# Kernel optimization log

Measured on AMD Instinct MI355X. Metric: run time of the kernel, lower is better.

## Reference

```python
import jax, jax.numpy as jnp
import numpy as np

EPS = 1e-12  # matches torch F.normalize default eps

def l2norm(t):
    n = jnp.linalg.norm(t, axis=-1, keepdims=True)
    return t / jnp.maximum(n, EPS)

def rotate_half(x):
    # '... (j d) -> ... j d' with j=2: split into two halves, return cat(-x2, x1)
    x1, x2 = jnp.split(x, 2, axis=-1)
    return jnp.concatenate((-x2, x1), axis=-1)

def rotary_freqs(seq_len, dim):
    inv_freq = 1.0 / (10000.0 ** (jnp.arange(0, dim, 2, dtype=jnp.float32) / dim))
    seq = jnp.arange(seq_len, dtype=jnp.float32)
    freqs = seq[:, None] * inv_freq[None, :]          # [n, d/2]
    emb = jnp.concatenate((freqs, freqs), axis=-1)    # [n, d]
    return emb[None, None]                            # [1, 1, n, d]

def apply_rotary_pos_emb(t, freqs):
    # rot_dim == dim_head here, so the pass-through slice is empty
    return t * jnp.cos(freqs) + rotate_half(t) * jnp.sin(freqs)

def setup_inputs() -> dict:
    key = jax.random.key(0)
    kq, kk, kv = jax.random.split(key, 3)
    b, h, n, d = 2, 16, 2048, 64
    q = jax.random.normal(kq, (b, h, n, d), dtype=jnp.float32)
    k = jax.random.normal(kk, (b, h, n, d), dtype=jnp.float32)
    v = jax.random.normal(kv, (b, h, n, d), dtype=jnp.float32)
    q_scale = jnp.ones((d,), dtype=jnp.float32)
    k_scale = jnp.ones((d,), dtype=jnp.float32)
    return {"q": q, "k": k, "v": v, "q_scale": q_scale, "k_scale": k_scale}

def reference(q, k, v, q_scale, k_scale):
    b, h, n, d = q.shape
    # QK RMSNorm (l2 normalize + learned per-dim scale)
    q = l2norm(q) * q_scale
    k = l2norm(k) * k_scale
    # rotary position embedding (always applied in the source module)
    freqs = rotary_freqs(n, d)
    q = apply_rotary_pos_emb(q, freqs)
    k = apply_rotary_pos_emb(k, freqs)
    # attention: explicit scores -> softmax -> values
    scale = d ** -0.5
    sim = jnp.einsum('bhid,bhjd->bhij', q, k) * scale
    attn = jax.nn.softmax(sim, axis=-1)
    out = jnp.einsum('bhij,bhjd->bhid', attn, v)
    # 'b h n d -> b n (h d)'
    return out.transpose(0, 2, 1, 3).reshape(b, n, h * d)
```

## Files before the change

### kernel.cpp

```cpp
#include <hip/hip_runtime.h>
#include <math.h>

#define BH   32
#define NSEQ 2048
#define DH   64
#define NH   16
#define LOG2E 1.44269504088896f

typedef _Float16 f16x8 __attribute__((ext_vector_type(8)));
typedef __fp16   fp16x2 __attribute__((ext_vector_type(2)));
typedef float    f32x16v __attribute__((ext_vector_type(16)));

#if __has_builtin(__builtin_amdgcn_exp2f)
#define EXP2F(x) __builtin_amdgcn_exp2f(x)
#else
#define EXP2F(x) exp2f(x)
#endif

static __device__ __forceinline__ unsigned pkrtz(float a, float b) {
    fp16x2 r = __builtin_amdgcn_cvt_pkrtz(a, b);
    return __builtin_bit_cast(unsigned, r);
}
static __device__ __forceinline__ unsigned packh_rne(float a, float b) {
    union { _Float16 h[2]; unsigned u; } x;
    x.h[0] = (_Float16)a; x.h[1] = (_Float16)b;
    return x.u;
}
#if __has_builtin(__builtin_amdgcn_perm)
#define PERM(a, b, s) __builtin_amdgcn_perm((a), (b), (s))
#else
static __device__ __forceinline__ unsigned PERM(unsigned a, unsigned b, unsigned s) {
    if (s == 0x05040100u) return (b & 0xffffu) | (a << 16);
    return (b >> 16) | (a & 0xffff0000u);
}
#endif

static __device__ __forceinline__ float2 rope_cs(int pos, int p) {
    float invf_rev = EXP2F(-(float)p * (13.287712379549449f / 32.0f)) * 0.15915494309189535f;
    float rev = (float)pos * invf_rev;
    float fr = rev - floorf(rev);
    float th = fr * 6.283185307179586f;
    return make_float2(__cosf(th), __sinf(th));
}

__global__ __launch_bounds__(256) void prep_all(
    const float* __restrict__ q, const float* __restrict__ k, const float* __restrict__ v,
    const float* __restrict__ qs, const float* __restrict__ ksc,
    unsigned* __restrict__ qh, unsigned* __restrict__ kh, unsigned* __restrict__ vt2) {
    const int bid = blockIdx.x;
    const int t = threadIdx.x;
    if (bid < 16384) {
        const bool isq = bid < 8192;
        const float* in = isq ? q : k;
        const float* sc = isq ? qs : ksc;
        unsigned* outp  = isq ? qh : kh;
        const float smul = isq ? 0.125f * LOG2E : 1.0f;
        const int sb = bid & 8191;
        const int w = t >> 6, lane = t & 63;
        const int c = lane & 31, hfr = lane >> 5;
        const int row = sb * 8 + w * 2 + hfr;
        float2 x2 = *(const float2*)(in + (size_t)row * DH + 2 * c);
        float ss = x2.x * x2.x + x2.y * x2.y;
        #pragma unroll
        for (int off = 16; off > 0; off >>= 1) ss += __shfl_xor(ss, off);
        float inv = 1.0f / fmaxf(sqrtf(ss), 1e-12f);
        float2 s2 = *(const float2*)(sc + 2 * c);
        float t0 = x2.x * inv * s2.x;
        float t1 = x2.y * inv * s2.y;
        float p0 = __shfl_xor(t0, 16);
        float p1 = __shfl_xor(t1, 16);
        float r0 = (c < 16) ? -p0 : p0;
        float r1 = (c < 16) ? -p1 : p1;
        int pos = row & (NSEQ - 1);
        int pp = (2 * c) & 31;
        float2 cs0 = rope_cs(pos, pp);
        float2 cs1 = rope_cs(pos, pp + 1);
        float o0 = (t0 * cs0.x + r0 * cs0.y) * smul;
        float o1 = (t1 * cs1.x + r1 * cs1.y) * smul;
        outp[row * 32 + c] = packh_rne(o0, o1);
    } else {
        const int sb = bid - 16384;
        const int kt = sb & 31, bh = sb >> 5;
        __shared__ float Lv[64 * 68];
        #pragma unroll
        for (int i = 0; i < 4; ++i) {
            int chunk = t + 256 * i;
            int r = chunk >> 4, fg = chunk & 15;
            *(float4*)&Lv[r * 68 + fg * 4] =
                *(const float4*)(v + ((size_t)bh * NSEQ + kt * 64 + r) * DH + fg * 4);
        }
        __syncthreads();
        const int dp = t >> 3, kg = t & 7;
        unsigned u[8];
        #pragma unroll
        for (int j = 0; j < 8; ++j) {
            int key = kg * 8 + j;
            float2 f2 = *(const float2*)&Lv[key * 68 + 2 * dp];
            u[j] = pkrtz(f2.x, f2.y);
        }
        unsigned* dst = vt2 + ((size_t)bh * 32 + dp) * NSEQ + kt * 64 + kg * 8;
        *(uint4*)(dst + 0) = make_uint4(u[0], u[1], u[2], u[3]);
        *(uint4*)(dst + 4) = make_uint4(u[4], u[5], u[6], u[7]);
    }
}

__global__ __launch_bounds__(128, 2) void attn_kernel(
    const unsigned* __restrict__ qh, const unsigned* __restrict__ khg,
    const unsigned* __restrict__ vt2, float* __restrict__ out) {

    __shared__ _Float16 Ks[2][64 * 72];
    __shared__ _Float16 Vs[2][64 * 72];

    const int bh = blockIdx.y, qb = blockIdx.x;
    const int tid = threadIdx.x;
    const int w = tid >> 6, lane = tid & 63;
    const int c = lane & 31, hf = lane >> 5;

    const _Float16* qbase = (const _Float16*)qh + ((size_t)bh * NSEQ + qb * 64) * DH;
    const _Float16* kbase = (const _Float16*)khg + (size_t)bh * NSEQ * DH;
    const unsigned* vbase = vt2 + (size_t)bh * 32 * NSEQ;

    #pragma unroll
    for (int i = 0; i < 4; ++i) {
        int chunk = tid + 128 * i;
        int r = chunk >> 3, sg = chunk & 7;
        *(uint4*)&Ks[0][r * 72 + sg * 8] = *(const uint4*)(kbase + r * DH + sg * 8);
    }
    #pragma unroll
    for (int i = 0; i < 4; ++i) {
        int chunk = tid + 128 * i;
        int dp = chunk >> 4, kq = (chunk & 15) * 4;
        uint4 vr = *(const uint4*)(vbase + (size_t)dp * NSEQ + kq);
        uint2 lo, hi;
        lo.x = PERM(vr.y, vr.x, 0x05040100u); hi.x = PERM(vr.y, vr.x, 0x07060302u);
        lo.y = PERM(vr.w, vr.z, 0x05040100u); hi.y = PERM(vr.w, vr.z, 0x07060302u);
        *(uint2*)&Vs[0][(2 * dp) * 72 + kq]     = lo;
        *(uint2*)&Vs[0][(2 * dp + 1) * 72 + kq] = hi;
    }

    f16x8 qf[4];
    #pragma unroll
    for (int ks = 0; ks < 4; ++ks)
        qf[ks] = *(const f16x8*)(qbase + (w * 32 + c) * DH + ks * 16 + hf * 8);

    f32x16v o[2];
    #pragma unroll
    for (int mt = 0; mt < 2; ++mt)
        #pragma unroll
        for (int r = 0; r < 16; ++r) o[mt][r] = 0.f;
    float lpart = 0.f;

    __syncthreads();

    for (int jt = 0; jt < 32; ++jt) {
        const int cur = jt & 1;
        uint4 kpre[4], vpre[4];
        if (jt + 1 < 32) {
            #pragma unroll
            for (int i = 0; i < 4; ++i) {
                int chunk = tid + 128 * i;
                int r = chunk >> 3, sg = chunk & 7;
                kpre[i] = *(const uint4*)(kbase + (size_t)(jt + 1) * 64 * DH + r * DH + sg * 8);
            }
            #pragma unroll
            for (int i = 0; i < 4; ++i) {
                int chunk = tid + 128 * i;
                int dp = chunk >> 4, kq = (chunk & 15) * 4;
                vpre[i] = *(const uint4*)(vbase + (size_t)dp * NSEQ + (jt + 1) * 64 + kq);
            }
        }

        f32x16v s[2];
        #pragma unroll
        for (int mt = 0; mt < 2; ++mt)
            #pragma unroll
            for (int r = 0; r < 16; ++r) s[mt][r] = 0.f;
        #pragma unroll
        for (int ks = 0; ks < 4; ++ks) {
            f16x8 ka0 = *(const f16x8*)&Ks[cur][c * 72 + ks * 16 + hf * 8];
            f16x8 ka1 = *(const f16x8*)&Ks[cur][(32 + c) * 72 + ks * 16 + hf * 8];
            s[0] = __builtin_amdgcn_mfma_f32_32x32x16_f16(ka0, qf[ks], s[0], 0, 0, 0);
            s[1] = __builtin_amdgcn_mfma_f32_32x32x16_f16(ka1, qf[ks], s[1], 0, 0, 0);
        }

        #pragma unroll
        for (int mt = 0; mt < 2; ++mt)
            #pragma unroll
            for (int r = 0; r < 16; ++r) {
                float pv = EXP2F(s[mt][r]);
                s[mt][r] = pv;
                lpart += pv;
            }

        #pragma unroll
        for (int mt = 0; mt < 2; ++mt) {
            #pragma unroll
            for (int kk = 0; kk < 2; ++kk) {
                unsigned P01 = pkrtz(s[mt][kk * 8 + 0], s[mt][kk * 8 + 1]);
                unsigned P23 = pkrtz(s[mt][kk * 8 + 2], s[mt][kk * 8 + 3]);
                unsigned P45 = pkrtz(s[mt][kk * 8 + 4], s[mt][kk * 8 + 5]);
                unsigned P67 = pkrtz(s[mt][kk * 8 + 6], s[mt][kk * 8 + 7]);
                unsigned x01 = (unsigned)__shfl_xor((int)P01, 32);
                unsigned x23 = (unsigned)__shfl_xor((int)P23, 32);
                unsigned x45 = (unsigned)__shfl_xor((int)P45, 32);
                unsigned x67 = (unsigned)__shfl_xor((int)P67, 32);
                union { unsigned u[4]; f16x8 v; } B;
                B.u[0] = hf ? x45 : P01;
                B.u[1] = hf ? x67 : P23;
                B.u[2] = hf ? P45 : x01;
                B.u[3] = hf ? P67 : x23;
                const int kc = mt * 2 + kk;
                f16x8 va0 = *(const f16x8*)&Vs[cur][c * 72 + kc * 16 + hf * 8];
                f16x8 va1 = *(const f16x8*)&Vs[cur][(32 + c) * 72 + kc * 16 + hf * 8];
                o[0] = __builtin_amdgcn_mfma_f32_32x32x16_f16(va0, B.v, o[0], 0, 0, 0);
                o[1] = __builtin_amdgcn_mfma_f32_32x32x16_f16(va1, B.v, o[1], 0, 0, 0);
            }
        }

        if (jt + 1 < 32) {
            #pragma unroll
            for (int i = 0; i < 4; ++i) {
                int chunk = tid + 128 * i;
                int r = chunk >> 3, sg = chunk & 7;
                *(uint4*)&Ks[1 - cur][r * 72 + sg * 8] = kpre[i];
            }
            #pragma unroll
            for (int i = 0; i < 4; ++i) {
                int chunk = tid + 128 * i;
                int dp = chunk >> 4, kq = (chunk & 15) * 4;
                uint2 lo, hi;
                lo.x = PERM(vpre[i].y, vpre[i].x, 0x05040100u); hi.x = PERM(vpre[i].y, vpre[i].x, 0x07060302u);
                lo.y = PERM(vpre[i].w, vpre[i].z, 0x05040100u); hi.y = PERM(vpre[i].w, vpre[i].z, 0x07060302u);
                *(uint2*)&Vs[1 - cur][(2 * dp) * 72 + kq]     = lo;
                *(uint2*)&Vs[1 - cur][(2 * dp + 1) * 72 + kq] = hi;
            }
        }
        __syncthreads();
    }

    float ltot = lpart + __shfl_xor(lpart, 32);
    float invl = 1.0f / ltot;
    const int b = bh >> 4, h = bh & 15;
    const int pos = qb * 64 + w * 32 + c;
    float* obase = out + ((size_t)b * NSEQ + pos) * (NH * DH) + h * DH;
    #pragma unroll
    for (int mt = 0; mt < 2; ++mt)
        #pragma unroll
        for (int g = 0; g < 4; ++g) {
            float4 r4 = make_float4(o[mt][g * 4 + 0] * invl, o[mt][g * 4 + 1] * invl,
                                    o[mt][g * 4 + 2] * invl, o[mt][g * 4 + 3] * invl);
            *(float4*)(obase + mt * 32 + g * 8 + hf * 4) = r4;
        }
}

extern "C" void kernel_launch(void* const* d_in, const int* in_sizes, int n_in,
                              void* d_out, int out_size, void* d_ws, size_t ws_size,
                              hipStream_t stream) {
    const float* q  = (const float*)d_in[0];
    const float* k  = (const float*)d_in[1];
    const float* v  = (const float*)d_in[2];
    const float* qs = (const float*)d_in[3];
    const float* ks = (const float*)d_in[4];
    float* outp = (float*)d_out;

    unsigned* qh  = (unsigned*)d_ws;
    unsigned* kh  = qh + (size_t)BH * NSEQ * 32;
    unsigned* vt2 = kh + (size_t)BH * NSEQ * 32;

    prep_all<<<17408, 256, 0, stream>>>(q, k, v, qs, ks, qh, kh, vt2);
    attn_kernel<<<dim3(NSEQ / 64, BH), 128, 0, stream>>>(qh, kh, vt2, outp);
}
```

Before: 153.6 us.

## Split key tiles across four waves with LDS reduction of partial outputs

Doubles the block to four waves. Each pair of waves processes half of every key tile for the same query rows, and the partial O and row sums are combined through shared memory at the end. This shortens each wave's serial MFMA/exp chain per tile and adds more waves for latency hiding. The cost is duplicated Q fragments and O accumulators, plus an extra reduction pass. The cross-half exchange of P also switches to permlane32_swap when available.

```diff
diff --git a/kernel.cpp b/kernel.cpp
--- a/kernel.cpp
+++ b/kernel.cpp
@@ -10,6 +10,7 @@
 typedef _Float16 f16x8 __attribute__((ext_vector_type(8)));
 typedef __fp16   fp16x2 __attribute__((ext_vector_type(2)));
 typedef float    f32x16v __attribute__((ext_vector_type(16)));
+typedef unsigned uint2v __attribute__((ext_vector_type(2)));
 
 #if __has_builtin(__builtin_amdgcn_exp2f)
 #define EXP2F(x) __builtin_amdgcn_exp2f(x)
@@ -104,7 +105,7 @@
     }
 }
 
-__global__ __launch_bounds__(128, 2) void attn_kernel(
+__global__ __launch_bounds__(256, 4) void attn_kernel(
     const unsigned* __restrict__ qh, const unsigned* __restrict__ khg,
     const unsigned* __restrict__ vt2, float* __restrict__ out) {
 
@@ -115,20 +116,22 @@
     const int tid = threadIdx.x;
     const int w = tid >> 6, lane = tid & 63;
     const int c = lane & 31, hf = lane >> 5;
+    const int qhw = w & 1;
+    const int khw = w >> 1;
 
     const _Float16* qbase = (const _Float16*)qh + ((size_t)bh * NSEQ + qb * 64) * DH;
     const _Float16* kbase = (const _Float16*)khg + (size_t)bh * NSEQ * DH;
     const unsigned* vbase = vt2 + (size_t)bh * 32 * NSEQ;
 
     #pragma unroll
-    for (int i = 0; i < 4; ++i) {
-        int chunk = tid + 128 * i;
+    for (int i = 0; i < 2; ++i) {
+        int chunk = tid + 256 * i;
         int r = chunk >> 3, sg = chunk & 7;
         *(uint4*)&Ks[0][r * 72 + sg * 8] = *(const uint4*)(kbase + r * DH + sg * 8);
     }
     #pragma unroll
-    for (int i = 0; i < 4; ++i) {
-        int chunk = tid + 128 * i;
+    for (int i = 0; i < 2; ++i) {
+        int chunk = tid + 256 * i;
         int dp = chunk >> 4, kq = (chunk & 15) * 4;
         uint4 vr = *(const uint4*)(vbase + (size_t)dp * NSEQ + kq);
         uint2 lo, hi;
@@ -141,7 +144,7 @@
     f16x8 qf[4];
     #pragma unroll
     for (int ks = 0; ks < 4; ++ks)
-        qf[ks] = *(const f16x8*)(qbase + (w * 32 + c) * DH + ks * 16 + hf * 8);
+        qf[ks] = *(const f16x8*)(qbase + (qhw * 32 + c) * DH + ks * 16 + hf * 8);
 
     f32x16v o[2];
     #pragma unroll
@@ -154,79 +157,76 @@
 
     for (int jt = 0; jt < 32; ++jt) {
         const int cur = jt & 1;
-        uint4 kpre[4], vpre[4];
+        uint4 kpre[2], vpre[2];
         if (jt + 1 < 32) {
             #pragma unroll
-            for (int i = 0; i < 4; ++i) {
-                int chunk = tid + 128 * i;
+            for (int i = 0; i < 2; ++i) {
+                int chunk = tid + 256 * i;
                 int r = chunk >> 3, sg = chunk & 7;
                 kpre[i] = *(const uint4*)(kbase + (size_t)(jt + 1) * 64 * DH + r * DH + sg * 8);
             }
             #pragma unroll
-            for (int i = 0; i < 4; ++i) {
-                int chunk = tid + 128 * i;
+            for (int i = 0; i < 2; ++i) {
+                int chunk = tid + 256 * i;
                 int dp = chunk >> 4, kq = (chunk & 15) * 4;
                 vpre[i] = *(const uint4*)(vbase + (size_t)dp * NSEQ + (jt + 1) * 64 + kq);
             }
         }
 
-        f32x16v s[2];
-        #pragma unroll
-        for (int mt = 0; mt < 2; ++mt)
-            #pragma unroll
-            for (int r = 0; r < 16; ++r) s[mt][r] = 0.f;
+        f32x16v s;
+        #pragma unroll
+        for (int r = 0; r < 16; ++r) s[r] = 0.f;
         #pragma unroll
         for (int ks = 0; ks < 4; ++ks) {
-            f16x8 ka0 = *(const f16x8*)&Ks[cur][c * 72 + ks * 16 + hf * 8];
-            f16x8 ka1 = *(const f16x8*)&Ks[cur][(32 + c) * 72 + ks * 16 + hf * 8];
-            s[0] = __builtin_amdgcn_mfma_f32_32x32x16_f16(ka0, qf[ks], s[0], 0, 0, 0);
-            s[1] = __builtin_amdgcn_mfma_f32_32x32x16_f16(ka1, qf[ks], s[1], 0, 0, 0);
-        }
-
-        #pragma unroll
-        for (int mt = 0; mt < 2; ++mt)
-            #pragma unroll
-            for (int r = 0; r < 16; ++r) {
-                float pv = EXP2F(s[mt][r]);
-                s[mt][r] = pv;
-                lpart += pv;
-            }
-
-        #pragma unroll
-        for (int mt = 0; mt < 2; ++mt) {
-            #pragma unroll
-            for (int kk = 0; kk < 2; ++kk) {
-                unsigned P01 = pkrtz(s[mt][kk * 8 + 0], s[mt][kk * 8 + 1]);
-                unsigned P23 = pkrtz(s[mt][kk * 8 + 2], s[mt][kk * 8 + 3]);
-                unsigned P45 = pkrtz(s[mt][kk * 8 + 4], s[mt][kk * 8 + 5]);
-                unsigned P67 = pkrtz(s[mt][kk * 8 + 6], s[mt][kk * 8 + 7]);
-                unsigned x01 = (unsigned)__shfl_xor((int)P01, 32);
-                unsigned x23 = (unsigned)__shfl_xor((int)P23, 32);
-                unsigned x45 = (unsigned)__shfl_xor((int)P45, 32);
-                unsigned x67 = (unsigned)__shfl_xor((int)P67, 32);
-                union { unsigned u[4]; f16x8 v; } B;
-                B.u[0] = hf ? x45 : P01;
-                B.u[1] = hf ? x67 : P23;
-                B.u[2] = hf ? P45 : x01;
-                B.u[3] = hf ? P67 : x23;
-                const int kc = mt * 2 + kk;
-                f16x8 va0 = *(const f16x8*)&Vs[cur][c * 72 + kc * 16 + hf * 8];
-                f16x8 va1 = *(const f16x8*)&Vs[cur][(32 + c) * 72 + kc * 16 + hf * 8];
-                o[0] = __builtin_amdgcn_mfma_f32_32x32x16_f16(va0, B.v, o[0], 0, 0, 0);
-                o[1] = __builtin_amdgcn_mfma_f32_32x32x16_f16(va1, B.v, o[1], 0, 0, 0);
-            }
+            f16x8 ka = *(const f16x8*)&Ks[cur][(khw * 32 + c) * 72 + ks * 16 + hf * 8];
+            s = __builtin_amdgcn_mfma_f32_32x32x16_f16(ka, qf[ks], s, 0, 0, 0);
+        }
+
+        #pragma unroll
+        for (int r = 0; r < 16; ++r) {
+            float pv = EXP2F(s[r]);
+            s[r] = pv;
+            lpart += pv;
+        }
+
+        #pragma unroll
+        for (int kk = 0; kk < 2; ++kk) {
+            unsigned P01 = pkrtz(s[kk * 8 + 0], s[kk * 8 + 1]);
+            unsigned P23 = pkrtz(s[kk * 8 + 2], s[kk * 8 + 3]);
+            unsigned P45 = pkrtz(s[kk * 8 + 4], s[kk * 8 + 5]);
+            unsigned P67 = pkrtz(s[kk * 8 + 6], s[kk * 8 + 7]);
+            union { unsigned u[4]; f16x8 v; } B;
+#if __has_builtin(__builtin_amdgcn_permlane32_swap)
+            uint2v r02 = __builtin_amdgcn_permlane32_swap(P01, P45, 0, 0);
+            uint2v r13 = __builtin_amdgcn_permlane32_swap(P23, P67, 0, 0);
+            B.u[0] = r02[0]; B.u[1] = r13[0]; B.u[2] = r02[1]; B.u[3] = r13[1];
+#else
+            unsigned x01 = (unsigned)__shfl_xor((int)P01, 32);
+            unsigned x23 = (unsigned)__shfl_xor((int)P23, 32);
+            unsigned x45 = (unsigned)__shfl_xor((int)P45, 32);
+            unsigned x67 = (unsigned)__shfl_xor((int)P67, 32);
+            B.u[0] = hf ? x45 : P01;
+            B.u[1] = hf ? x67 : P23;
+            B.u[2] = hf ? P45 : x01;
+            B.u[3] = hf ? P67 : x23;
+#endif
+            const int kc = khw * 2 + kk;
+            f16x8 va0 = *(const f16x8*)&Vs[cur][c * 72 + kc * 16 + hf * 8];
+            f16x8 va1 = *(const f16x8*)&Vs[cur][(32 + c) * 72 + kc * 16 + hf * 8];
+            o[0] = __builtin_amdgcn_mfma_f32_32x32x16_f16(va0, B.v, o[0], 0, 0, 0);
+            o[1] = __builtin_amdgcn_mfma_f32_32x32x16_f16(va1, B.v, o[1], 0, 0, 0);
         }
 
         if (jt + 1 < 32) {
             #pragma unroll
-            for (int i = 0; i < 4; ++i) {
-                int chunk = tid + 128 * i;
+            for (int i = 0; i < 2; ++i) {
+                int chunk = tid + 256 * i;
                 int r = chunk >> 3, sg = chunk & 7;
                 *(uint4*)&Ks[1 - cur][r * 72 + sg * 8] = kpre[i];
             }
             #pragma unroll
-            for (int i = 0; i < 4; ++i) {
-                int chunk = tid + 128 * i;
+            for (int i = 0; i < 2; ++i) {
+                int chunk = tid + 256 * i;
                 int dp = chunk >> 4, kq = (chunk & 15) * 4;
                 uint2 lo, hi;
                 lo.x = PERM(vpre[i].y, vpre[i].x, 0x05040100u); hi.x = PERM(vpre[i].y, vpre[i].x, 0x07060302u);
@@ -238,19 +238,37 @@
         __syncthreads();
     }
 
-    float ltot = lpart + __shfl_xor(lpart, 32);
-    float invl = 1.0f / ltot;
-    const int b = bh >> 4, h = bh & 15;
-    const int pos = qb * 64 + w * 32 + c;
-    float* obase = out + ((size_t)b * NSEQ + pos) * (NH * DH) + h * DH;
-    #pragma unroll
-    for (int mt = 0; mt < 2; ++mt)
-        #pragma unroll
-        for (int g = 0; g < 4; ++g) {
-            float4 r4 = make_float4(o[mt][g * 4 + 0] * invl, o[mt][g * 4 + 1] * invl,
-                                    o[mt][g * 4 + 2] * invl, o[mt][g * 4 + 3] * invl);
-            *(float4*)(obase + mt * 32 + g * 8 + hf * 4) = r4;
-        }
+    float lw = lpart + __shfl_xor(lpart, 32);
+    float* Lred = (float*)&Ks[0][0];
+    if (w >= 2) {
+        const int base = ((w - 2) * 64 + lane) * 33;
+        #pragma unroll
+        for (int mt = 0; mt < 2; ++mt)
+            #pragma unroll
+            for (int r = 0; r < 16; ++r) Lred[base + mt * 16 + r] = o[mt][r];
+        Lred[base + 32] = lw;
+    }
+    __syncthreads();
+    if (w < 2) {
+        const int base = (w * 64 + lane) * 33;
+        #pragma unroll
+        for (int mt = 0; mt < 2; ++mt)
+            #pragma unroll
+            for (int r = 0; r < 16; ++r) o[mt][r] += Lred[base + mt * 16 + r];
+        lw += Lred[base + 32];
+        float invl = 1.0f / lw;
+        const int b = bh >> 4, h = bh & 15;
+        const int pos = qb * 64 + w * 32 + c;
+        float* obase = out + ((size_t)b * NSEQ + pos) * (NH * DH) + h * DH;
+        #pragma unroll
+        for (int mt = 0; mt < 2; ++mt)
+            #pragma unroll
+            for (int g = 0; g < 4; ++g) {
+                float4 r4 = make_float4(o[mt][g * 4 + 0] * invl, o[mt][g * 4 + 1] * invl,
+                                        o[mt][g * 4 + 2] * invl, o[mt][g * 4 + 3] * invl);
+                *(float4*)(obase + mt * 32 + g * 8 + hf * 4) = r4;
+            }
+    }
 }
 
 extern "C" void kernel_launch(void* const* d_in, const int* in_sizes, int n_in,
@@ -268,5 +286,5 @@
     unsigned* vt2 = kh + (size_t)BH * NSEQ * 32;
 
     prep_all<<<17408, 256, 0, stream>>>(q, k, v, qs, ks, qh, kh, vt2);
-    attn_kernel<<<dim3(NSEQ / 64, BH), 128, 0, stream>>>(qh, kh, vt2, outp);
-}
+    attn_kernel<<<dim3(NSEQ / 64, BH), 256, 0, stream>>>(qh, kh, vt2, outp);
+}
```

After: 149.0 us. 1.03x faster.
